# Kernel tuning notes

Measured on AMD Instinct MI355X. Metric: run time of the kernel, lower is better.

Reference implementation:

```python
import jax, jax.numpy as jnp
import numpy as np
import math

L, V, D, H, T, B = 12, 50257, 1024, 16, 1024, 1
HD = D // H
EPS = 1e-5


def layernorm(x, g, b):
    m = jnp.mean(x, axis=-1, keepdims=True)
    v = jnp.var(x, axis=-1, keepdims=True)
    return (x - m) * jax.lax.rsqrt(v + EPS) * g + b


def gelu_tanh(x):
    return 0.5 * x * (1.0 + jnp.tanh(math.sqrt(2.0 / math.pi) * (x + 0.044715 * x ** 3)))


def setup_inputs() -> dict:
    key = jax.random.key(0)
    ks = jax.random.split(key, 16)
    s = 0.02
    inp = {
        "x": jax.random.randint(ks[0], (B, T), 0, V),
        "attention_mask": jnp.ones((B, T), jnp.float32),
        "tok_emb": jax.random.normal(ks[1], (V, D), jnp.float32) * s,
        "pos_emb": jax.random.normal(ks[2], (T, D), jnp.float32) * s,
        "ln1_g": jnp.ones((L, D), jnp.float32),
        "ln1_b": jnp.zeros((L, D), jnp.float32),
        "qkv_w": jax.random.normal(ks[3], (L, D, 3 * D), jnp.float32) * s,
        "qkv_b": jnp.zeros((L, 3 * D), jnp.float32),
        "out_w": jax.random.normal(ks[4], (L, D, D), jnp.float32) * s,
        "out_b": jnp.zeros((L, D), jnp.float32),
        "ln2_g": jnp.ones((L, D), jnp.float32),
        "ln2_b": jnp.zeros((L, D), jnp.float32),
        "fc1_w": jax.random.normal(ks[5], (L, D, 4 * D), jnp.float32) * s,
        "fc1_b": jnp.zeros((L, 4 * D), jnp.float32),
        "fc2_w": jax.random.normal(ks[6], (L, 4 * D, D), jnp.float32) * s,
        "fc2_b": jnp.zeros((L, D), jnp.float32),
        "lnf_g": jnp.ones((D,), jnp.float32),
        "lnf_b": jnp.zeros((D,), jnp.float32),
        "lm_w": jax.random.normal(ks[7], (V, D), jnp.float32) * s,
    }
    return inp


def reference(x, attention_mask, tok_emb, pos_emb, ln1_g, ln1_b, qkv_w, qkv_b,
              out_w, out_b, ln2_g, ln2_b, fc1_w, fc1_b, fc2_w, fc2_b,
              lnf_g, lnf_b, lm_w):
    Bx, Tx = x.shape
    h = tok_emb[x] + pos_emb[:Tx]  # (B,T,D)
    causal = jnp.tril(jnp.ones((Tx, Tx), bool))  # (T,T)
    amask_add = (1.0 - attention_mask)[:, None, None, :] * jnp.finfo(h.dtype).min
    scale = 1.0 / math.sqrt(HD)

    def block(h, p):
        l1g, l1b, qw, qb, ow, ob, l2g, l2b, f1w, f1b, f2w, f2b = p
        xn = layernorm(h, l1g, l1b)
        qkv = xn @ qw + qb  # (B,T,3D)
        q, k, v = jnp.split(qkv, 3, axis=-1)
        q = q.reshape(Bx, Tx, H, HD).transpose(0, 2, 1, 3)  # (B,H,T,hd)
        k = k.reshape(Bx, Tx, H, HD).transpose(0, 2, 1, 3)
        v = v.reshape(Bx, Tx, H, HD).transpose(0, 2, 1, 3)
        att = jnp.einsum('bhqd,bhkd->bhqk', q, k) * scale
        att = jnp.where(causal, att, -jnp.inf)
        att = att + amask_add
        att = jax.nn.softmax(att, axis=-1)
        wv = jnp.einsum('bhqk,bhkd->bhqd', att, v)
        wv = wv.transpose(0, 2, 1, 3).reshape(Bx, Tx, D)
        h = h + (wv @ ow + ob)
        xn2 = layernorm(h, l2g, l2b)
        ff = gelu_tanh(xn2 @ f1w + f1b) @ f2w + f2b
        return h + ff, None

    params = (ln1_g, ln1_b, qkv_w, qkv_b, out_w, out_b,
              ln2_g, ln2_b, fc1_w, fc1_b, fc2_w, fc2_b)
    h, _ = jax.lax.scan(block, h, params)
    h = layernorm(h, lnf_g, lnf_b)
    logits = jnp.einsum('btd,vd->btv', h, lm_w)
    return logits
```

## Files before the change

### kernel.cpp

```cpp
#include <hip/hip_runtime.h>
#include <hip/hip_bf16.h>
#include <math.h>

#define Lnum 12
#define Tn 1024
#define Dm 1024
#define Hn 16
#define HDn 64
#define Vn 50257

typedef __bf16 bf16;
typedef __bf16 bf16x4 __attribute__((ext_vector_type(4)));
typedef __bf16 bf16x8 __attribute__((ext_vector_type(8)));
typedef float f32x4 __attribute__((ext_vector_type(4)));

__device__ __forceinline__ void gload_lds16(const void* g, void* l) {
    __builtin_amdgcn_global_load_lds(
        (const __attribute__((address_space(1))) void*)g,
        (__attribute__((address_space(3))) void*)l, 16, 0, 0);
}

__device__ __forceinline__ float gelu_f(float x) {
    const float c = 0.7978845608028654f;
    return 0.5f * x * (1.0f + tanhf(c * (x + 0.044715f * x * x * x)));
}

__global__ __launch_bounds__(256) void embed_k(const int* __restrict__ x,
                                               const float* __restrict__ tok,
                                               const float* __restrict__ pos,
                                               float* __restrict__ h) {
    int t = blockIdx.x;
    int id = x[t];
    const float4* tr = (const float4*)(tok + (size_t)id * Dm);
    const float4* pr = (const float4*)(pos + (size_t)t * Dm);
    float4* hr = (float4*)(h + (size_t)t * Dm);
    int i = threadIdx.x;
    float4 a = tr[i], b = pr[i];
    hr[i] = make_float4(a.x + b.x, a.y + b.y, a.z + b.z, a.w + b.w);
}

__global__ __launch_bounds__(256) void cvt_k(const float* __restrict__ in,
                                             bf16* __restrict__ out, int n8) {
    int stride = gridDim.x * 256;
    for (int i = blockIdx.x * 256 + threadIdx.x; i < n8; i += stride) {
        float4 f0 = ((const float4*)in)[i * 2];
        float4 f1 = ((const float4*)in)[i * 2 + 1];
        bf16x8 pk;
        pk[0] = (bf16)f0.x; pk[1] = (bf16)f0.y; pk[2] = (bf16)f0.z; pk[3] = (bf16)f0.w;
        pk[4] = (bf16)f1.x; pk[5] = (bf16)f1.y; pk[6] = (bf16)f1.z; pk[7] = (bf16)f1.w;
        *(bf16x8*)(out + (size_t)i * 8) = pk;
    }
}

__global__ __launch_bounds__(256) void ln_k(const float* __restrict__ x,
                                            const float* __restrict__ g,
                                            const float* __restrict__ b,
                                            bf16* __restrict__ y) {
    int row = blockIdx.x;
    int tid = threadIdx.x;
    const float* xr = x + (size_t)row * Dm;
    float4 v = ((const float4*)xr)[tid];
    float s = v.x + v.y + v.z + v.w;
    float s2 = v.x * v.x + v.y * v.y + v.z * v.z + v.w * v.w;
    __shared__ float rs[256], rs2[256];
    rs[tid] = s; rs2[tid] = s2;
    __syncthreads();
    for (int off = 128; off; off >>= 1) {
        if (tid < off) { rs[tid] += rs[tid + off]; rs2[tid] += rs2[tid + off]; }
        __syncthreads();
    }
    float mean = rs[0] * (1.0f / Dm);
    float var = rs2[0] * (1.0f / Dm) - mean * mean;
    float inv = rsqrtf(var + 1e-5f);
    float4 gg = ((const float4*)g)[tid];
    float4 bb = ((const float4*)b)[tid];
    bf16x4 pk;
    pk[0] = (bf16)((v.x - mean) * inv * gg.x + bb.x);
    pk[1] = (bf16)((v.y - mean) * inv * gg.y + bb.y);
    pk[2] = (bf16)((v.z - mean) * inv * gg.z + bb.z);
    pk[3] = (bf16)((v.w - mean) * inv * gg.w + bb.w);
    *(bf16x4*)(y + (size_t)row * Dm + tid * 4) = pk;
}

__global__ __launch_bounds__(256) void tconv4_k(const float* __restrict__ qw,
                                                const float* __restrict__ ow,
                                                const float* __restrict__ f1,
                                                const float* __restrict__ f2,
                                                bf16* __restrict__ qT, bf16* __restrict__ oT,
                                                bf16* __restrict__ f1T, bf16* __restrict__ f2T) {
    int blk = blockIdx.x;
    const float* W; bf16* WT; int K, N, bi;
    if (blk < 3072)      { W = qw; WT = qT;  K = 1024; N = 3072; bi = blk; }
    else if (blk < 4096) { W = ow; WT = oT;  K = 1024; N = 1024; bi = blk - 3072; }
    else if (blk < 8192) { W = f1; WT = f1T; K = 1024; N = 4096; bi = blk - 4096; }
    else                 { W = f2; WT = f2T; K = 4096; N = 1024; bi = blk - 8192; }
    int nx = N >> 5;
    int n0 = (bi % nx) * 32;
    int k0 = (bi / nx) * 32;
    __shared__ float t[32][33];
    int tx = threadIdx.x & 31, ty = threadIdx.x >> 5;
#pragma unroll
    for (int r = 0; r < 4; ++r)
        t[ty + r * 8][tx] = W[(size_t)(k0 + ty + r * 8) * N + n0 + tx];
    __syncthreads();
    int row = threadIdx.x >> 3;
    int k4 = (threadIdx.x & 7) * 4;
    bf16x4 pk;
#pragma unroll
    for (int j = 0; j < 4; ++j) pk[j] = (bf16)t[k4 + j][row];
    *(bf16x4*)(WT + (size_t)(n0 + row) * K + k0 + k4) = pk;
}

template <int BM, int BN, int ACT, bool RESID, bool OUTBF, int BMODE, bool NTAIL>
__global__ __launch_bounds__(256) void mgemm_k(const bf16* __restrict__ A,
                                               const void* __restrict__ Btv,
                                               const float* __restrict__ bias,
                                               const float* __restrict__ resid,
                                               void* __restrict__ Cv,
                                               int N, int K, int nbm, int nbn) {
    constexpr int MI = BM / 32;
    constexpr int NJ = BN / 32;
    __shared__ bf16 As[BM * 64];
    __shared__ bf16 Bs[BN * 64];
    const int tid = threadIdx.x;
    const int lane = tid & 63;
    const int wid = tid >> 6;

    const int bfl = blockIdx.x;
    const int xcd = bfl & 7;
    const int t1 = bfl >> 3;
    const int rr = t1 % nbm;
    const int cg = t1 / nbm;
    const int bm = rr * BM;
    const int bn = (cg * 8 + xcd) * BN;

    const int wr = (wid >> 1) * (BM / 2);
    const int wc = (wid & 1) * (BN / 2);
    const int l15 = lane & 15;
    const int l4 = lane >> 4;

    f32x4 acc[MI][NJ] = {};

    for (int k0 = 0; k0 < K; k0 += 64) {
#pragma unroll
        for (int u = 0; u < BM / 32; ++u) {
            int ch = u * 256 + tid;
            int row = ch >> 3;
            int cb = (ch & 7) * 16;
            int ksw = (cb ^ ((row & 7) << 4)) >> 1;
            gload_lds16(A + (size_t)(bm + row) * K + k0 + ksw, &As[u * 2048 + wid * 512]);
        }
        if (BMODE == 0) {
            const bf16* B = (const bf16*)Btv;
#pragma unroll
            for (int u = 0; u < BN / 32; ++u) {
                int ch = u * 256 + tid;
                int row = ch >> 3;
                int cb = (ch & 7) * 16;
                int ksw = (cb ^ ((row & 7) << 4)) >> 1;
                gload_lds16(B + (size_t)(bn + row) * K + k0 + ksw, &Bs[u * 2048 + wid * 512]);
            }
        } else {
            const float* B = (const float*)Btv;
#pragma unroll
            for (int it = 0; it < BN / 32; ++it) {
                int gi = it * 256 + tid;
                int row = gi >> 3;
                int cb = (gi & 7) * 16;
                int n = bn + row;
                if (NTAIL && n >= N) n = N - 1;
                const float* g = B + (size_t)n * K + k0 + (gi & 7) * 8;
                float4 f0 = *(const float4*)g;
                float4 f1 = *(const float4*)(g + 4);
                bf16x8 pk;
                pk[0] = (bf16)f0.x; pk[1] = (bf16)f0.y; pk[2] = (bf16)f0.z; pk[3] = (bf16)f0.w;
                pk[4] = (bf16)f1.x; pk[5] = (bf16)f1.y; pk[6] = (bf16)f1.z; pk[7] = (bf16)f1.w;
                *(bf16x8*)((char*)Bs + row * 128 + (cb ^ ((row & 7) << 4))) = pk;
            }
        }
        __syncthreads();

#pragma unroll
        for (int kk = 0; kk < 2; ++kk) {
            const int kb = kk * 64 + l4 * 16;
            bf16x8 a[MI], b[NJ];
#pragma unroll
            for (int i = 0; i < MI; ++i) {
                int row = wr + i * 16 + l15;
                a[i] = *(const bf16x8*)((char*)As + row * 128 + (kb ^ ((row & 7) << 4)));
            }
#pragma unroll
            for (int j = 0; j < NJ; ++j) {
                int row = wc + j * 16 + l15;
                b[j] = *(const bf16x8*)((char*)Bs + row * 128 + (kb ^ ((row & 7) << 4)));
            }
#pragma unroll
            for (int i = 0; i < MI; ++i)
#pragma unroll
                for (int j = 0; j < NJ; ++j)
                    acc[i][j] = __builtin_amdgcn_mfma_f32_16x16x32_bf16(a[i], b[j], acc[i][j], 0, 0, 0);
        }
        __syncthreads();
    }

#pragma unroll
    for (int i = 0; i < MI; ++i) {
        int row0 = bm + wr + i * 16 + l4 * 4;
#pragma unroll
        for (int j = 0; j < NJ; ++j) {
            int col = bn + wc + j * 16 + l15;
            if (NTAIL && col >= N) continue;
            float bv = bias ? bias[col] : 0.f;
#pragma unroll
            for (int r = 0; r < 4; ++r) {
                float v = acc[i][j][r] + bv;
                if (ACT == 1) v = gelu_f(v);
                size_t idx = (size_t)(row0 + r) * N + col;
                if (RESID) v += resid[idx];
                if (OUTBF) ((bf16*)Cv)[idx] = (bf16)v;
                else       ((float*)Cv)[idx] = v;
            }
        }
    }
}

__global__ __launch_bounds__(128) void fattn_k(const bf16* __restrict__ qkv,
                                               const float* __restrict__ amask,
                                               bf16* __restrict__ out) {
    __shared__ bf16 Ks[64 * 64];
    __shared__ bf16 Vt[64 * 64];
    __shared__ bf16 Pw[2][16 * 64];
    __shared__ float addb[Tn];
    __shared__ float bcast[2][16];

    const int f = blockIdx.x;
    const int hh = f & 15;
    const int s = f >> 4;
    const int qt = (s < 16) ? s : 47 - s;
    const int tid = threadIdx.x;
    const int lane = tid & 63;
    const int wq = tid >> 6;
    const int l15 = lane & 15;
    const int g = lane >> 4;

    const int qglob = qt * 32 + wq * 16 + l15;
    const int nkt = (qt >> 1) + 1;
    const int kmax = nkt * 64;

    for (int i = tid; i < kmax; i += 128)
        addb[i] = (1.0f - amask[i]) * -3.0e38f;

    bf16x8 qreg[2];
    {
        const bf16* qp = qkv + (size_t)qglob * (3 * Dm) + hh * HDn + g * 8;
        qreg[0] = *(const bf16x8*)qp;
        qreg[1] = *(const bf16x8*)(qp + 32);
    }

    f32x4 accO[4] = {};
    float mrun = -3.0e38f, lrun = 0.f;

    for (int kt = 0; kt < nkt; ++kt) {
        const int kb = kt * 64;
        __syncthreads();
#pragma unroll
        for (int t2 = 0; t2 < 4; ++t2) {
            int c = tid + t2 * 128;
            int kr = c >> 3;
            int d8 = (c & 7) * 8;
            const bf16* gp = qkv + (size_t)(kb + kr) * (3 * Dm) + Dm + hh * HDn + d8;
            bf16x8 v = *(const bf16x8*)gp;
            *(bf16x8*)((char*)Ks + kr * 128 + ((d8 * 2) ^ ((kr & 7) << 4))) = v;
        }
#pragma unroll
        for (int t2 = 0; t2 < 4; ++t2) {
            int c = tid + t2 * 128;
            int k = c >> 3, d0 = (c & 7) * 8;
            const bf16* gp = qkv + (size_t)(kb + k) * (3 * Dm) + 2 * Dm + hh * HDn + d0;
            bf16x8 v = *(const bf16x8*)gp;
#pragma unroll
            for (int j = 0; j < 8; ++j) {
                int d = d0 + j;
                *(bf16*)((char*)Vt + d * 128 + ((2 * k) ^ ((d & 7) << 4))) = v[j];
            }
        }
        __syncthreads();

        f32x4 accS[4] = {};
        __builtin_amdgcn_s_setprio(1);
#pragma unroll
        for (int s2 = 0; s2 < 2; ++s2)
#pragma unroll
            for (int mf = 0; mf < 4; ++mf) {
                int kr = mf * 16 + l15;
                bf16x8 af = *(const bf16x8*)((char*)Ks + kr * 128 + ((s2 * 64 + g * 16) ^ ((kr & 7) << 4)));
                accS[mf] = __builtin_amdgcn_mfma_f32_16x16x32_bf16(af, qreg[s2], accS[mf], 0, 0, 0);
            }
        __builtin_amdgcn_s_setprio(0);

        float p[16];
        float tmax = -3.0e38f;
#pragma unroll
        for (int mf = 0; mf < 4; ++mf)
#pragma unroll
            for (int r = 0; r < 4; ++r) {
                int k = kb + mf * 16 + g * 4 + r;
                float sv = accS[mf][r] * 0.125f + addb[k];
                if (k > qglob) sv = -3.0e38f;
                p[mf * 4 + r] = sv;
                tmax = fmaxf(tmax, sv);
            }
        tmax = fmaxf(tmax, __shfl_xor(tmax, 16, 64));
        tmax = fmaxf(tmax, __shfl_xor(tmax, 32, 64));
        float mnew = fmaxf(mrun, tmax);
        float alpha = expf(mrun - mnew);
        float psum = 0.f;
#pragma unroll
        for (int i = 0; i < 16; ++i) { float e = expf(p[i] - mnew); p[i] = e; psum += e; }
        psum += __shfl_xor(psum, 16, 64);
        psum += __shfl_xor(psum, 32, 64);
        lrun = lrun * alpha + psum;
        mrun = mnew;

        if (g == 0) bcast[wq][l15] = alpha;
        f32x4 av = *(f32x4*)&bcast[wq][g * 4];
#pragma unroll
        for (int nf = 0; nf < 4; ++nf)
#pragma unroll
            for (int r = 0; r < 4; ++r) accO[nf][r] *= av[r];

        char* pw = (char*)Pw[wq];
#pragma unroll
        for (int mf = 0; mf < 4; ++mf) {
            bf16x4 pk;
            pk[0] = (bf16)p[mf * 4 + 0]; pk[1] = (bf16)p[mf * 4 + 1];
            pk[2] = (bf16)p[mf * 4 + 2]; pk[3] = (bf16)p[mf * 4 + 3];
            *(bf16x4*)(pw + l15 * 128 + ((32 * mf + 8 * g) ^ ((l15 & 7) << 4))) = pk;
        }
        bf16x8 pa[2];
#pragma unroll
        for (int s2 = 0; s2 < 2; ++s2)
            pa[s2] = *(const bf16x8*)(pw + l15 * 128 + ((s2 * 64 + g * 16) ^ ((l15 & 7) << 4)));

        __builtin_amdgcn_s_setprio(1);
#pragma unroll
        for (int s2 = 0; s2 < 2; ++s2)
#pragma unroll
            for (int nf = 0; nf < 4; ++nf) {
                int d = nf * 16 + l15;
                bf16x8 bfg = *(const bf16x8*)((char*)Vt + d * 128 + ((s2 * 64 + g * 16) ^ ((d & 7) << 4)));
                accO[nf] = __builtin_amdgcn_mfma_f32_16x16x32_bf16(pa[s2], bfg, accO[nf], 0, 0, 0);
            }
        __builtin_amdgcn_s_setprio(0);
    }

    if (g == 0) bcast[wq][l15] = 1.0f / lrun;
    f32x4 lv = *(f32x4*)&bcast[wq][g * 4];
#pragma unroll
    for (int nf = 0; nf < 4; ++nf)
#pragma unroll
        for (int r = 0; r < 4; ++r) {
            int row = qt * 32 + wq * 16 + 4 * g + r;
            int col = hh * HDn + nf * 16 + l15;
            out[(size_t)row * Dm + col] = (bf16)(accO[nf][r] * lv[r]);
        }
}

extern "C" void kernel_launch(void* const* d_in, const int* in_sizes, int n_in,
                              void* d_out, int out_size, void* d_ws, size_t ws_size,
                              hipStream_t stream) {
    const int*   x      = (const int*)d_in[0];
    const float* amask  = (const float*)d_in[1];
    const float* tok    = (const float*)d_in[2];
    const float* pos    = (const float*)d_in[3];
    const float* ln1_g  = (const float*)d_in[4];
    const float* ln1_b  = (const float*)d_in[5];
    const float* qkv_w  = (const float*)d_in[6];
    const float* qkv_b  = (const float*)d_in[7];
    const float* out_w  = (const float*)d_in[8];
    const float* out_b  = (const float*)d_in[9];
    const float* ln2_g  = (const float*)d_in[10];
    const float* ln2_b  = (const float*)d_in[11];
    const float* fc1_w  = (const float*)d_in[12];
    const float* fc1_b  = (const float*)d_in[13];
    const float* fc2_w  = (const float*)d_in[14];
    const float* fc2_b  = (const float*)d_in[15];
    const float* lnf_g  = (const float*)d_in[16];
    const float* lnf_b  = (const float*)d_in[17];
    const float* lm_w   = (const float*)d_in[18];

    char* ws = (char*)d_ws;
    float* h      = (float*)(ws + 0);
    bf16*  qkv_bf = (bf16*) (ws + (4u << 20));
    bf16*  xn_bf  = (bf16*) (ws + (16u << 20));
    bf16*  wv_bf  = (bf16*) (ws + (18u << 20));
    bf16*  ff1_bf = (bf16*) (ws + (20u << 20));
    bf16*  Wbuf   = (bf16*) (ws + (28u << 20));
    bf16* qT  = Wbuf;
    bf16* oT  = qT  + 3145728;
    bf16* f1T = oT  + 1048576;
    bf16* f2T = f1T + 4194304;
    bf16* lm_bf = (bf16*)(ws + (52u << 20));
    float* outf = (float*)d_out;

    const bool big_ws = ws_size >= ((size_t)153 << 20);

    embed_k<<<Tn, 256, 0, stream>>>(x, tok, pos, h);

    for (int l = 0; l < Lnum; ++l) {
        const float* l1g = ln1_g + (size_t)l * Dm;
        const float* l1b = ln1_b + (size_t)l * Dm;
        const float* qw  = qkv_w + (size_t)l * Dm * 3 * Dm;
        const float* qb  = qkv_b + (size_t)l * 3 * Dm;
        const float* ow  = out_w + (size_t)l * Dm * Dm;
        const float* ob  = out_b + (size_t)l * Dm;
        const float* l2g = ln2_g + (size_t)l * Dm;
        const float* l2b = ln2_b + (size_t)l * Dm;
        const float* f1w = fc1_w + (size_t)l * Dm * 4 * Dm;
        const float* f1b = fc1_b + (size_t)l * 4 * Dm;
        const float* f2w = fc2_w + (size_t)l * 4 * Dm * Dm;
        const float* f2b = fc2_b + (size_t)l * Dm;

        tconv4_k<<<12288, 256, 0, stream>>>(qw, ow, f1w, f2w, qT, oT, f1T, f2T);
        ln_k<<<Tn, 256, 0, stream>>>(h, l1g, l1b, xn_bf);
        mgemm_k<64, 64, 0, false, true, 0, false><<<768, 256, 0, stream>>>(
            xn_bf, qT, qb, nullptr, qkv_bf, 3 * Dm, Dm, 16, 48);
        fattn_k<<<512, 128, 0, stream>>>(qkv_bf, amask, wv_bf);
        mgemm_k<32, 64, 0, true, false, 0, false><<<512, 256, 0, stream>>>(
            wv_bf, oT, ob, h, h, Dm, Dm, 32, 16);
        ln_k<<<Tn, 256, 0, stream>>>(h, l2g, l2b, xn_bf);
        mgemm_k<64, 64, 1, false, true, 0, false><<<1024, 256, 0, stream>>>(
            xn_bf, f1T, f1b, nullptr, ff1_bf, 4 * Dm, Dm, 16, 64);
        mgemm_k<32, 64, 0, true, false, 0, false><<<512, 256, 0, stream>>>(
            ff1_bf, f2T, f2b, h, h, Dm, 4 * Dm, 32, 16);
    }

    ln_k<<<Tn, 256, 0, stream>>>(h, lnf_g, lnf_b, xn_bf);
    if (big_ws) {
        cvt_k<<<2048, 256, 0, stream>>>(lm_w, lm_bf, (Vn * Dm) / 8);
        mgemm_k<128, 128, 0, false, false, 0, true><<<8 * 400, 256, 0, stream>>>(
            xn_bf, lm_bf, nullptr, nullptr, outf, Vn, Dm, 8, 400);
    } else {
        mgemm_k<128, 128, 0, false, false, 1, true><<<8 * 400, 256, 0, stream>>>(
            xn_bf, lm_w, nullptr, nullptr, outf, Vn, Dm, 8, 400);
    }
}
```

Before: 1.865 ms.

## Replace 4-wave layer GEMMs with single-wave 16x16x32 MFMA GEMM kernel

Adds a single-wavefront GEMM kernel (64 threads per block) that loads a BMx64 A tile and a 64x64 B tile per K step through swizzled direct-to-LDS loads, then uses 16x16x32 bf16 MFMAs with raised wave priority. All four per-layer GEMMs (QKV, out-proj, FC1 with GELU, FC2) switch to it with the same grid sizes. The aim is to cut block-level barrier overhead and raise occupancy by giving each block one wave. In exchange there is no double buffering, each wave owns the whole tile, and every K step waits on vmcnt(0) with no load/compute overlap.

```diff
diff --git a/kernel.cpp b/kernel.cpp
--- a/kernel.cpp
+++ b/kernel.cpp
@@ -109,6 +109,93 @@
 #pragma unroll
     for (int j = 0; j < 4; ++j) pk[j] = (bf16)t[k4 + j][row];
     *(bf16x4*)(WT + (size_t)(n0 + row) * K + k0 + k4) = pk;
+}
+
+template <int BM, int ACT, bool RESID, bool OUTBF>
+__global__ __launch_bounds__(64) void wgemm_k(const bf16* __restrict__ A,
+                                              const bf16* __restrict__ Bt,
+                                              const float* __restrict__ bias,
+                                              const float* __restrict__ resid,
+                                              void* __restrict__ Cv,
+                                              int N, int K, int nbm, int nbn) {
+    constexpr int MI = BM / 16;
+    __shared__ bf16 As[BM * 64];
+    __shared__ bf16 Bs[64 * 64];
+    const int lane = threadIdx.x;
+    const int l15 = lane & 15;
+    const int l4 = lane >> 4;
+
+    const int bfl = blockIdx.x;
+    const int xcd = bfl & 7;
+    const int t1 = bfl >> 3;
+    const int rr = t1 % nbm;
+    const int cg = t1 / nbm;
+    const int bm = rr * BM;
+    const int bn = (cg * 8 + xcd) * 64;
+
+    f32x4 acc[MI][4] = {};
+
+    for (int k0 = 0; k0 < K; k0 += 64) {
+#pragma unroll
+        for (int u = 0; u < BM / 8; ++u) {
+            int c = u * 64 + lane;
+            int row = c >> 3;
+            int cb = (c & 7) * 16;
+            int ksw = (cb ^ ((row & 7) << 4)) >> 1;
+            gload_lds16(A + (size_t)(bm + row) * K + k0 + ksw, &As[u * 512]);
+        }
+#pragma unroll
+        for (int u = 0; u < 8; ++u) {
+            int c = u * 64 + lane;
+            int row = c >> 3;
+            int cb = (c & 7) * 16;
+            int ksw = (cb ^ ((row & 7) << 4)) >> 1;
+            gload_lds16(Bt + (size_t)(bn + row) * K + k0 + ksw, &Bs[u * 512]);
+        }
+        asm volatile("s_waitcnt vmcnt(0)" ::: "memory");
+
+        __builtin_amdgcn_s_setprio(1);
+#pragma unroll
+        for (int kk = 0; kk < 2; ++kk) {
+            const int kb = kk * 64 + l4 * 16;
+            bf16x8 a[MI], b[4];
+#pragma unroll
+            for (int i = 0; i < MI; ++i) {
+                int row = i * 16 + l15;
+                a[i] = *(const bf16x8*)((char*)As + row * 128 + (kb ^ ((row & 7) << 4)));
+            }
+#pragma unroll
+            for (int j = 0; j < 4; ++j) {
+                int row = j * 16 + l15;
+                b[j] = *(const bf16x8*)((char*)Bs + row * 128 + (kb ^ ((row & 7) << 4)));
+            }
+#pragma unroll
+            for (int i = 0; i < MI; ++i)
+#pragma unroll
+                for (int j = 0; j < 4; ++j)
+                    acc[i][j] = __builtin_amdgcn_mfma_f32_16x16x32_bf16(a[i], b[j], acc[i][j], 0, 0, 0);
+        }
+        __builtin_amdgcn_s_setprio(0);
+    }
+
+#pragma unroll
+    for (int i = 0; i < MI; ++i) {
+        int row0 = bm + i * 16 + l4 * 4;
+#pragma unroll
+        for (int j = 0; j < 4; ++j) {
+            int col = bn + j * 16 + l15;
+            float bv = bias ? bias[col] : 0.f;
+#pragma unroll
+            for (int r = 0; r < 4; ++r) {
+                float v = acc[i][j][r] + bv;
+                if (ACT == 1) v = gelu_f(v);
+                size_t idx = (size_t)(row0 + r) * N + col;
+                if (RESID) v += resid[idx];
+                if (OUTBF) ((bf16*)Cv)[idx] = (bf16)v;
+                else       ((float*)Cv)[idx] = v;
+            }
+        }
+    }
 }
 
 template <int BM, int BN, int ACT, bool RESID, bool OUTBF, int BMODE, bool NTAIL>
@@ -423,15 +510,15 @@
 
         tconv4_k<<<12288, 256, 0, stream>>>(qw, ow, f1w, f2w, qT, oT, f1T, f2T);
         ln_k<<<Tn, 256, 0, stream>>>(h, l1g, l1b, xn_bf);
-        mgemm_k<64, 64, 0, false, true, 0, false><<<768, 256, 0, stream>>>(
+        wgemm_k<64, 0, false, true><<<768, 64, 0, stream>>>(
             xn_bf, qT, qb, nullptr, qkv_bf, 3 * Dm, Dm, 16, 48);
         fattn_k<<<512, 128, 0, stream>>>(qkv_bf, amask, wv_bf);
-        mgemm_k<32, 64, 0, true, false, 0, false><<<512, 256, 0, stream>>>(
+        wgemm_k<32, 0, true, false><<<512, 64, 0, stream>>>(
             wv_bf, oT, ob, h, h, Dm, Dm, 32, 16);
         ln_k<<<Tn, 256, 0, stream>>>(h, l2g, l2b, xn_bf);
-        mgemm_k<64, 64, 1, false, true, 0, false><<<1024, 256, 0, stream>>>(
+        wgemm_k<64, 1, false, true><<<1024, 64, 0, stream>>>(
             xn_bf, f1T, f1b, nullptr, ff1_bf, 4 * Dm, Dm, 16, 64);
-        mgemm_k<32, 64, 0, true, false, 0, false><<<512, 256, 0, stream>>>(
+        wgemm_k<32, 0, true, false><<<512, 64, 0, stream>>>(
             ff1_bf, f2T, f2b, h, h, Dm, 4 * Dm, 32, 16);
     }
 
```

Result: slower. 2.201 ms (+18.0%).

## Double-buffer LDS tiles in per-layer GEMMs with vmcnt-based prefetch

Applied to the files above, without the earlier changes.

Adds a DBUF template path to the MFMA GEMM that stages the next K-tile into a second LDS buffer via global_load_lds while computing on the current one. It waits with explicit s_waitcnt vmcnt on the outstanding loads, which removes one barrier per iteration. The aim is to overlap global-to-LDS transfer with MFMA work in the per-layer QKV, out-proj, FC1 and FC2 GEMMs. The cost is double the LDS use, which may lower occupancy. Correctness relies on the vmcnt counts and a single barrier being enough cross-wave synchronisation for the LDS writes.

```diff
diff --git a/kernel.cpp b/kernel.cpp
--- a/kernel.cpp
+++ b/kernel.cpp
@@ -18,6 +18,13 @@
     __builtin_amdgcn_global_load_lds(
         (const __attribute__((address_space(1))) void*)g,
         (__attribute__((address_space(3))) void*)l, 16, 0, 0);
+}
+
+template <int N> __device__ __forceinline__ void waitcnt_vm() {
+    if constexpr (N == 0)      asm volatile("s_waitcnt vmcnt(0)" ::: "memory");
+    else if constexpr (N == 3) asm volatile("s_waitcnt vmcnt(3)" ::: "memory");
+    else if constexpr (N == 4) asm volatile("s_waitcnt vmcnt(4)" ::: "memory");
+    else if constexpr (N == 8) asm volatile("s_waitcnt vmcnt(8)" ::: "memory");
 }
 
 __device__ __forceinline__ float gelu_f(float x) {
@@ -111,7 +118,7 @@
     *(bf16x4*)(WT + (size_t)(n0 + row) * K + k0 + k4) = pk;
 }
 
-template <int BM, int BN, int ACT, bool RESID, bool OUTBF, int BMODE, bool NTAIL>
+template <int BM, int BN, int ACT, bool RESID, bool OUTBF, int BMODE, bool NTAIL, bool DBUF>
 __global__ __launch_bounds__(256) void mgemm_k(const bf16* __restrict__ A,
                                                const void* __restrict__ Btv,
                                                const float* __restrict__ bias,
@@ -120,8 +127,10 @@
                                                int N, int K, int nbm, int nbn) {
     constexpr int MI = BM / 32;
     constexpr int NJ = BN / 32;
-    __shared__ bf16 As[BM * 64];
-    __shared__ bf16 Bs[BN * 64];
+    constexpr int NBUF = DBUF ? 2 : 1;
+    constexpr int NV = BM / 32 + BN / 32;
+    __shared__ bf16 As[NBUF * BM * 64];
+    __shared__ bf16 Bs[NBUF * BN * 64];
     const int tid = threadIdx.x;
     const int lane = tid & 63;
     const int wid = tid >> 6;
@@ -141,45 +150,31 @@
 
     f32x4 acc[MI][NJ] = {};
 
-    for (int k0 = 0; k0 < K; k0 += 64) {
+    auto stage_bf = [&](int half, int k0) {
 #pragma unroll
         for (int u = 0; u < BM / 32; ++u) {
             int ch = u * 256 + tid;
             int row = ch >> 3;
             int cb = (ch & 7) * 16;
             int ksw = (cb ^ ((row & 7) << 4)) >> 1;
-            gload_lds16(A + (size_t)(bm + row) * K + k0 + ksw, &As[u * 2048 + wid * 512]);
-        }
-        if (BMODE == 0) {
-            const bf16* B = (const bf16*)Btv;
-#pragma unroll
-            for (int u = 0; u < BN / 32; ++u) {
-                int ch = u * 256 + tid;
-                int row = ch >> 3;
-                int cb = (ch & 7) * 16;
-                int ksw = (cb ^ ((row & 7) << 4)) >> 1;
-                gload_lds16(B + (size_t)(bn + row) * K + k0 + ksw, &Bs[u * 2048 + wid * 512]);
-            }
-        } else {
-            const float* B = (const float*)Btv;
-#pragma unroll
-            for (int it = 0; it < BN / 32; ++it) {
-                int gi = it * 256 + tid;
-                int row = gi >> 3;
-                int cb = (gi & 7) * 16;
-                int n = bn + row;
-                if (NTAIL && n >= N) n = N - 1;
-                const float* g = B + (size_t)n * K + k0 + (gi & 7) * 8;
-                float4 f0 = *(const float4*)g;
-                float4 f1 = *(const float4*)(g + 4);
-                bf16x8 pk;
-                pk[0] = (bf16)f0.x; pk[1] = (bf16)f0.y; pk[2] = (bf16)f0.z; pk[3] = (bf16)f0.w;
-                pk[4] = (bf16)f1.x; pk[5] = (bf16)f1.y; pk[6] = (bf16)f1.z; pk[7] = (bf16)f1.w;
-                *(bf16x8*)((char*)Bs + row * 128 + (cb ^ ((row & 7) << 4))) = pk;
-            }
-        }
-        __syncthreads();
-
+            gload_lds16(A + (size_t)(bm + row) * K + k0 + ksw,
+                        &As[half * BM * 64 + u * 2048 + wid * 512]);
+        }
+        const bf16* B = (const bf16*)Btv;
+#pragma unroll
+        for (int u = 0; u < BN / 32; ++u) {
+            int ch = u * 256 + tid;
+            int row = ch >> 3;
+            int cb = (ch & 7) * 16;
+            int ksw = (cb ^ ((row & 7) << 4)) >> 1;
+            gload_lds16(B + (size_t)(bn + row) * K + k0 + ksw,
+                        &Bs[half * BN * 64 + u * 2048 + wid * 512]);
+        }
+    };
+
+    auto compute = [&](int half) {
+        const char* aB = (const char*)&As[half * BM * 64];
+        const char* bB = (const char*)&Bs[half * BN * 64];
 #pragma unroll
         for (int kk = 0; kk < 2; ++kk) {
             const int kb = kk * 64 + l4 * 16;
@@ -187,12 +182,12 @@
 #pragma unroll
             for (int i = 0; i < MI; ++i) {
                 int row = wr + i * 16 + l15;
-                a[i] = *(const bf16x8*)((char*)As + row * 128 + (kb ^ ((row & 7) << 4)));
+                a[i] = *(const bf16x8*)(aB + row * 128 + (kb ^ ((row & 7) << 4)));
             }
 #pragma unroll
             for (int j = 0; j < NJ; ++j) {
                 int row = wc + j * 16 + l15;
-                b[j] = *(const bf16x8*)((char*)Bs + row * 128 + (kb ^ ((row & 7) << 4)));
+                b[j] = *(const bf16x8*)(bB + row * 128 + (kb ^ ((row & 7) << 4)));
             }
 #pragma unroll
             for (int i = 0; i < MI; ++i)
@@ -200,7 +195,57 @@
                 for (int j = 0; j < NJ; ++j)
                     acc[i][j] = __builtin_amdgcn_mfma_f32_16x16x32_bf16(a[i], b[j], acc[i][j], 0, 0, 0);
         }
-        __syncthreads();
+    };
+
+    if constexpr (DBUF) {
+        const int nt = K >> 6;
+        stage_bf(0, 0);
+        int cur = 0;
+        for (int t = 0; t < nt; ++t) {
+            if (t + 1 < nt) {
+                stage_bf(cur ^ 1, (t + 1) << 6);
+                waitcnt_vm<NV>();
+            } else {
+                waitcnt_vm<0>();
+            }
+            compute(cur);
+            __syncthreads();
+            cur ^= 1;
+        }
+    } else {
+        for (int k0 = 0; k0 < K; k0 += 64) {
+            if (BMODE == 0) {
+                stage_bf(0, k0);
+            } else {
+                const float* B = (const float*)Btv;
+#pragma unroll
+                for (int u = 0; u < BM / 32; ++u) {
+                    int ch = u * 256 + tid;
+                    int row = ch >> 3;
+                    int cb = (ch & 7) * 16;
+                    int ksw = (cb ^ ((row & 7) << 4)) >> 1;
+                    gload_lds16(A + (size_t)(bm + row) * K + k0 + ksw, &As[u * 2048 + wid * 512]);
+                }
+#pragma unroll
+                for (int it = 0; it < BN / 32; ++it) {
+                    int gi = it * 256 + tid;
+                    int row = gi >> 3;
+                    int cb = (gi & 7) * 16;
+                    int n = bn + row;
+                    if (NTAIL && n >= N) n = N - 1;
+                    const float* g = B + (size_t)n * K + k0 + (gi & 7) * 8;
+                    float4 f0 = *(const float4*)g;
+                    float4 f1 = *(const float4*)(g + 4);
+                    bf16x8 pk;
+                    pk[0] = (bf16)f0.x; pk[1] = (bf16)f0.y; pk[2] = (bf16)f0.z; pk[3] = (bf16)f0.w;
+                    pk[4] = (bf16)f1.x; pk[5] = (bf16)f1.y; pk[6] = (bf16)f1.z; pk[7] = (bf16)f1.w;
+                    *(bf16x8*)((char*)Bs + row * 128 + (cb ^ ((row & 7) << 4))) = pk;
+                }
+            }
+            __syncthreads();
+            compute(0);
+            __syncthreads();
+        }
     }
 
 #pragma unroll
@@ -423,25 +468,25 @@
 
         tconv4_k<<<12288, 256, 0, stream>>>(qw, ow, f1w, f2w, qT, oT, f1T, f2T);
         ln_k<<<Tn, 256, 0, stream>>>(h, l1g, l1b, xn_bf);
-        mgemm_k<64, 64, 0, false, true, 0, false><<<768, 256, 0, stream>>>(
+        mgemm_k<64, 64, 0, false, true, 0, false, true><<<768, 256, 0, stream>>>(
             xn_bf, qT, qb, nullptr, qkv_bf, 3 * Dm, Dm, 16, 48);
         fattn_k<<<512, 128, 0, stream>>>(qkv_bf, amask, wv_bf);
-        mgemm_k<32, 64, 0, true, false, 0, false><<<512, 256, 0, stream>>>(
+        mgemm_k<32, 64, 0, true, false, 0, false, true><<<512, 256, 0, stream>>>(
             wv_bf, oT, ob, h, h, Dm, Dm, 32, 16);
         ln_k<<<Tn, 256, 0, stream>>>(h, l2g, l2b, xn_bf);
-        mgemm_k<64, 64, 1, false, true, 0, false><<<1024, 256, 0, stream>>>(
+        mgemm_k<64, 64, 1, false, true, 0, false, true><<<1024, 256, 0, stream>>>(
             xn_bf, f1T, f1b, nullptr, ff1_bf, 4 * Dm, Dm, 16, 64);
-        mgemm_k<32, 64, 0, true, false, 0, false><<<512, 256, 0, stream>>>(
+        mgemm_k<32, 64, 0, true, false, 0, false, true><<<512, 256, 0, stream>>>(
             ff1_bf, f2T, f2b, h, h, Dm, 4 * Dm, 32, 16);
     }
 
     ln_k<<<Tn, 256, 0, stream>>>(h, lnf_g, lnf_b, xn_bf);
     if (big_ws) {
         cvt_k<<<2048, 256, 0, stream>>>(lm_w, lm_bf, (Vn * Dm) / 8);
-        mgemm_k<128, 128, 0, false, false, 0, true><<<8 * 400, 256, 0, stream>>>(
+        mgemm_k<128, 128, 0, false, false, 0, true, false><<<8 * 400, 256, 0, stream>>>(
             xn_bf, lm_bf, nullptr, nullptr, outf, Vn, Dm, 8, 400);
     } else {
-        mgemm_k<128, 128, 0, false, false, 1, true><<<8 * 400, 256, 0, stream>>>(
+        mgemm_k<128, 128, 0, false, false, 1, true, false><<<8 * 400, 256, 0, stream>>>(
             xn_bf, lm_w, nullptr, nullptr, outf, Vn, Dm, 8, 400);
     }
 }
```

Result: no change. 1.883 ms (+1.0%).

## Batch all-layer weight transposes upfront and deepen GEMM K-tile to 128

Applied to the files above, without the earlier changes.

When the workspace is large enough, one launch now converts and transposes every layer's fp32 weights to bf16 before the layer loop, instead of a separate conversion launch per layer. The lm_head bf16 buffer moves to a new offset to make room. Separately, the GEMM kernel gains a BK template parameter, and the per-layer GEMMs use a 128-wide K tile with a matching LDS swizzle. This halves K-loop iterations and barriers, but doubles shared memory per block, which may reduce occupancy. The batched-transpose path depends on the harness providing about 442 MB of workspace.

```diff
diff --git a/kernel.cpp b/kernel.cpp
--- a/kernel.cpp
+++ b/kernel.cpp
@@ -82,6 +82,23 @@
     *(bf16x4*)(y + (size_t)row * Dm + tid * 4) = pk;
 }
 
+__device__ __forceinline__ void tconv_body(const float* __restrict__ W,
+                                           bf16* __restrict__ WT,
+                                           int K, int N, int n0, int k0) {
+    __shared__ float t[32][33];
+    int tx = threadIdx.x & 31, ty = threadIdx.x >> 5;
+#pragma unroll
+    for (int r = 0; r < 4; ++r)
+        t[ty + r * 8][tx] = W[(size_t)(k0 + ty + r * 8) * N + n0 + tx];
+    __syncthreads();
+    int row = threadIdx.x >> 3;
+    int k4 = (threadIdx.x & 7) * 4;
+    bf16x4 pk;
+#pragma unroll
+    for (int j = 0; j < 4; ++j) pk[j] = (bf16)t[k4 + j][row];
+    *(bf16x4*)(WT + (size_t)(n0 + row) * K + k0 + k4) = pk;
+}
+
 __global__ __launch_bounds__(256) void tconv4_k(const float* __restrict__ qw,
                                                 const float* __restrict__ ow,
                                                 const float* __restrict__ f1,
@@ -95,23 +112,28 @@
     else if (blk < 8192) { W = f1; WT = f1T; K = 1024; N = 4096; bi = blk - 4096; }
     else                 { W = f2; WT = f2T; K = 4096; N = 1024; bi = blk - 8192; }
     int nx = N >> 5;
-    int n0 = (bi % nx) * 32;
-    int k0 = (bi / nx) * 32;
-    __shared__ float t[32][33];
-    int tx = threadIdx.x & 31, ty = threadIdx.x >> 5;
-#pragma unroll
-    for (int r = 0; r < 4; ++r)
-        t[ty + r * 8][tx] = W[(size_t)(k0 + ty + r * 8) * N + n0 + tx];
-    __syncthreads();
-    int row = threadIdx.x >> 3;
-    int k4 = (threadIdx.x & 7) * 4;
-    bf16x4 pk;
-#pragma unroll
-    for (int j = 0; j < 4; ++j) pk[j] = (bf16)t[k4 + j][row];
-    *(bf16x4*)(WT + (size_t)(n0 + row) * K + k0 + k4) = pk;
-}
-
-template <int BM, int BN, int ACT, bool RESID, bool OUTBF, int BMODE, bool NTAIL>
+    tconv_body(W, WT, K, N, (bi % nx) * 32, (bi / nx) * 32);
+}
+
+__global__ __launch_bounds__(256) void tconv_all_k(const float* __restrict__ qw0,
+                                                   const float* __restrict__ ow0,
+                                                   const float* __restrict__ f10,
+                                                   const float* __restrict__ f20,
+                                                   bf16* __restrict__ Wall) {
+    int blk = blockIdx.x;
+    int l = blk / 12288;
+    int bi0 = blk % 12288;
+    bf16* base = Wall + (size_t)l * 12582912;
+    const float* W; bf16* WT; int K, N, bi;
+    if (bi0 < 3072)      { W = qw0 + (size_t)l * 3145728; WT = base;           K = 1024; N = 3072; bi = bi0; }
+    else if (bi0 < 4096) { W = ow0 + (size_t)l * 1048576; WT = base + 3145728; K = 1024; N = 1024; bi = bi0 - 3072; }
+    else if (bi0 < 8192) { W = f10 + (size_t)l * 4194304; WT = base + 4194304; K = 1024; N = 4096; bi = bi0 - 4096; }
+    else                 { W = f20 + (size_t)l * 4194304; WT = base + 8388608; K = 4096; N = 1024; bi = bi0 - 8192; }
+    int nx = N >> 5;
+    tconv_body(W, WT, K, N, (bi % nx) * 32, (bi / nx) * 32);
+}
+
+template <int BM, int BN, int BK, int ACT, bool RESID, bool OUTBF, int BMODE, bool NTAIL>
 __global__ __launch_bounds__(256) void mgemm_k(const bf16* __restrict__ A,
                                                const void* __restrict__ Btv,
                                                const float* __restrict__ bias,
@@ -120,8 +142,11 @@
                                                int N, int K, int nbm, int nbn) {
     constexpr int MI = BM / 32;
     constexpr int NJ = BN / 32;
-    __shared__ bf16 As[BM * 64];
-    __shared__ bf16 Bs[BN * 64];
+    constexpr int CPR = BK / 8;
+    constexpr int CM = CPR - 1;
+    constexpr int RB = BK * 2;
+    __shared__ bf16 As[BM * BK];
+    __shared__ bf16 Bs[BN * BK];
     const int tid = threadIdx.x;
     const int lane = tid & 63;
     const int wid = tid >> 6;
@@ -141,58 +166,58 @@
 
     f32x4 acc[MI][NJ] = {};
 
-    for (int k0 = 0; k0 < K; k0 += 64) {
-#pragma unroll
-        for (int u = 0; u < BM / 32; ++u) {
+    for (int k0 = 0; k0 < K; k0 += BK) {
+#pragma unroll
+        for (int u = 0; u < BM * BK / 2048; ++u) {
             int ch = u * 256 + tid;
-            int row = ch >> 3;
-            int cb = (ch & 7) * 16;
-            int ksw = (cb ^ ((row & 7) << 4)) >> 1;
+            int row = ch / CPR;
+            int cb = (ch & CM) * 16;
+            int ksw = (cb ^ ((row & CM) << 4)) >> 1;
             gload_lds16(A + (size_t)(bm + row) * K + k0 + ksw, &As[u * 2048 + wid * 512]);
         }
         if (BMODE == 0) {
             const bf16* B = (const bf16*)Btv;
 #pragma unroll
-            for (int u = 0; u < BN / 32; ++u) {
+            for (int u = 0; u < BN * BK / 2048; ++u) {
                 int ch = u * 256 + tid;
-                int row = ch >> 3;
-                int cb = (ch & 7) * 16;
-                int ksw = (cb ^ ((row & 7) << 4)) >> 1;
+                int row = ch / CPR;
+                int cb = (ch & CM) * 16;
+                int ksw = (cb ^ ((row & CM) << 4)) >> 1;
                 gload_lds16(B + (size_t)(bn + row) * K + k0 + ksw, &Bs[u * 2048 + wid * 512]);
             }
         } else {
             const float* B = (const float*)Btv;
 #pragma unroll
-            for (int it = 0; it < BN / 32; ++it) {
+            for (int it = 0; it < BN * BK / 2048; ++it) {
                 int gi = it * 256 + tid;
-                int row = gi >> 3;
-                int cb = (gi & 7) * 16;
+                int row = gi / CPR;
+                int cb = (gi & CM) * 16;
                 int n = bn + row;
                 if (NTAIL && n >= N) n = N - 1;
-                const float* g = B + (size_t)n * K + k0 + (gi & 7) * 8;
+                const float* g = B + (size_t)n * K + k0 + (gi & CM) * 8;
                 float4 f0 = *(const float4*)g;
                 float4 f1 = *(const float4*)(g + 4);
                 bf16x8 pk;
                 pk[0] = (bf16)f0.x; pk[1] = (bf16)f0.y; pk[2] = (bf16)f0.z; pk[3] = (bf16)f0.w;
                 pk[4] = (bf16)f1.x; pk[5] = (bf16)f1.y; pk[6] = (bf16)f1.z; pk[7] = (bf16)f1.w;
-                *(bf16x8*)((char*)Bs + row * 128 + (cb ^ ((row & 7) << 4))) = pk;
+                *(bf16x8*)((char*)Bs + row * RB + (cb ^ ((row & CM) << 4))) = pk;
             }
         }
         __syncthreads();
 
 #pragma unroll
-        for (int kk = 0; kk < 2; ++kk) {
+        for (int kk = 0; kk < BK / 32; ++kk) {
             const int kb = kk * 64 + l4 * 16;
             bf16x8 a[MI], b[NJ];
 #pragma unroll
             for (int i = 0; i < MI; ++i) {
                 int row = wr + i * 16 + l15;
-                a[i] = *(const bf16x8*)((char*)As + row * 128 + (kb ^ ((row & 7) << 4)));
+                a[i] = *(const bf16x8*)((char*)As + row * RB + (kb ^ ((row & CM) << 4)));
             }
 #pragma unroll
             for (int j = 0; j < NJ; ++j) {
                 int row = wc + j * 16 + l15;
-                b[j] = *(const bf16x8*)((char*)Bs + row * 128 + (kb ^ ((row & 7) << 4)));
+                b[j] = *(const bf16x8*)((char*)Bs + row * RB + (kb ^ ((row & CM) << 4)));
             }
 #pragma unroll
             for (int i = 0; i < MI; ++i)
@@ -396,16 +421,18 @@
     bf16*  wv_bf  = (bf16*) (ws + (18u << 20));
     bf16*  ff1_bf = (bf16*) (ws + (20u << 20));
     bf16*  Wbuf   = (bf16*) (ws + (28u << 20));
-    bf16* qT  = Wbuf;
-    bf16* oT  = qT  + 3145728;
-    bf16* f1T = oT  + 1048576;
-    bf16* f2T = f1T + 4194304;
-    bf16* lm_bf = (bf16*)(ws + (52u << 20));
+    bf16*  Wall   = (bf16*) (ws + (52u << 20));
     float* outf = (float*)d_out;
 
-    const bool big_ws = ws_size >= ((size_t)153 << 20);
+    const bool huge_ws = ws_size >= ((size_t)442 << 20);
+    const bool big_ws  = ws_size >= ((size_t)153 << 20);
+    bf16* lm_bf = huge_ws ? (bf16*)(ws + (340u << 20))
+                          : (bf16*)(ws + (52u << 20));
 
     embed_k<<<Tn, 256, 0, stream>>>(x, tok, pos, h);
+
+    if (huge_ws)
+        tconv_all_k<<<12 * 12288, 256, 0, stream>>>(qkv_w, out_w, fc1_w, fc2_w, Wall);
 
     for (int l = 0; l < Lnum; ++l) {
         const float* l1g = ln1_g + (size_t)l * Dm;
@@ -421,27 +448,35 @@
         const float* f2w = fc2_w + (size_t)l * 4 * Dm * Dm;
         const float* f2b = fc2_b + (size_t)l * Dm;
 
-        tconv4_k<<<12288, 256, 0, stream>>>(qw, ow, f1w, f2w, qT, oT, f1T, f2T);
+        bf16 *qT, *oT, *f1T, *f2T;
+        if (huge_ws) {
+            bf16* base = Wall + (size_t)l * 12582912;
+            qT = base; oT = base + 3145728; f1T = base + 4194304; f2T = base + 8388608;
+        } else {
+            qT = Wbuf; oT = qT + 3145728; f1T = oT + 1048576; f2T = f1T + 4194304;
+            tconv4_k<<<12288, 256, 0, stream>>>(qw, ow, f1w, f2w, qT, oT, f1T, f2T);
+        }
+
         ln_k<<<Tn, 256, 0, stream>>>(h, l1g, l1b, xn_bf);
-        mgemm_k<64, 64, 0, false, true, 0, false><<<768, 256, 0, stream>>>(
+        mgemm_k<64, 64, 128, 0, false, true, 0, false><<<768, 256, 0, stream>>>(
             xn_bf, qT, qb, nullptr, qkv_bf, 3 * Dm, Dm, 16, 48);
         fattn_k<<<512, 128, 0, stream>>>(qkv_bf, amask, wv_bf);
-        mgemm_k<32, 64, 0, true, false, 0, false><<<512, 256, 0, stream>>>(
+        mgemm_k<32, 64, 128, 0, true, false, 0, false><<<512, 256, 0, stream>>>(
             wv_bf, oT, ob, h, h, Dm, Dm, 32, 16);
         ln_k<<<Tn, 256, 0, stream>>>(h, l2g, l2b, xn_bf);
-        mgemm_k<64, 64, 1, false, true, 0, false><<<1024, 256, 0, stream>>>(
+        mgemm_k<64, 64, 128, 1, false, true, 0, false><<<1024, 256, 0, stream>>>(
             xn_bf, f1T, f1b, nullptr, ff1_bf, 4 * Dm, Dm, 16, 64);
-        mgemm_k<32, 64, 0, true, false, 0, false><<<512, 256, 0, stream>>>(
+        mgemm_k<32, 64, 128, 0, true, false, 0, false><<<512, 256, 0, stream>>>(
             ff1_bf, f2T, f2b, h, h, Dm, 4 * Dm, 32, 16);
     }
 
     ln_k<<<Tn, 256, 0, stream>>>(h, lnf_g, lnf_b, xn_bf);
     if (big_ws) {
         cvt_k<<<2048, 256, 0, stream>>>(lm_w, lm_bf, (Vn * Dm) / 8);
-        mgemm_k<128, 128, 0, false, false, 0, true><<<8 * 400, 256, 0, stream>>>(
+        mgemm_k<128, 128, 64, 0, false, false, 0, true><<<8 * 400, 256, 0, stream>>>(
             xn_bf, lm_bf, nullptr, nullptr, outf, Vn, Dm, 8, 400);
     } else {
-        mgemm_k<128, 128, 0, false, false, 1, true><<<8 * 400, 256, 0, stream>>>(
+        mgemm_k<128, 128, 64, 0, false, false, 1, true><<<8 * 400, 256, 0, stream>>>(
             xn_bf, lm_w, nullptr, nullptr, outf, Vn, Dm, 8, 400);
     }
 }
```

Result: slower. 1.975 ms (+5.9%).
